# Performance work log

Hardware: AMD Instinct MI355X
Metric: run time of the kernel (lower is better)

## Reference

```python
import jax, jax.numpy as jnp
import numpy as np

SEQ, BATCH, IN, HID, OUT = 512, 64, 512, 1024, 512
KEEP = 0.7  # dropout p = 0.3


def setup_inputs() -> dict:
    key = jax.random.key(0)
    ks = jax.random.split(key, 9)
    def lin(k, fan_out, fan_in):
        bound = 1.0 / np.sqrt(fan_in)
        kw, kb = jax.random.split(k)
        W = jax.random.uniform(kw, (fan_out, fan_in), jnp.float32, -bound, bound)
        b = jax.random.uniform(kb, (fan_out,), jnp.float32, -bound, bound)
        return W, b
    x = jax.random.normal(ks[0], (SEQ, BATCH, IN), jnp.float32)
    # inverted dropout mask, fixed for determinism
    drop_mask = (jax.random.bernoulli(ks[1], KEEP, (SEQ, BATCH, OUT))
                 .astype(jnp.float32) / KEEP)
    W_i2h, b_i2h = lin(ks[2], HID, IN + HID)
    W_i2o, b_i2o = lin(ks[3], OUT, IN + HID)
    W_o2o, b_o2o = lin(ks[4], OUT, HID + OUT)
    return {"x": x, "drop_mask": drop_mask,
            "W_i2h": W_i2h, "b_i2h": b_i2h,
            "W_i2o": W_i2o, "b_i2o": b_i2o,
            "W_o2o": W_o2o, "b_o2o": b_o2o}


def reference(x, drop_mask, W_i2h, b_i2h, W_i2o, b_i2o, W_o2o, b_o2o):
    # x: [S, B, IN]; returns log-probs [S, B, OUT]
    def step(h, inp):
        x_t, m_t = inp  # [B, IN], [B, OUT]
        comb = jnp.concatenate([x_t, h], axis=1)          # [B, IN+HID]
        out = comb @ W_i2o.T + b_i2o                      # [B, OUT]
        h_new = comb @ W_i2h.T + b_i2h                    # [B, HID]
        oc = jnp.concatenate([out, h_new], axis=1) @ W_o2o.T + b_o2o  # [B, OUT]
        oc = oc * m_t                                     # dropout (inverted mask)
        oc = jax.nn.log_softmax(oc, axis=-1)
        return h_new, oc
    h0 = jnp.zeros((x.shape[1], W_i2h.shape[0]), x.dtype)
    _, outs = jax.lax.scan(step, h0, (x, drop_mask))
    return outs
```

## Files before the change

### kernel.cpp

```cpp
#include <hip/hip_runtime.h>
#include <stdint.h>
#include <string.h>


typedef unsigned short ushort_t;
typedef __attribute__((ext_vector_type(8))) __bf16 bf16x8;
typedef __attribute__((ext_vector_type(4))) float f32x4;

__device__ __forceinline__ ushort_t f2bf(float f) {
  union { float f; uint32_t u; } v; v.f = f;
  uint32_t r = v.u + 0x7fffu + ((v.u >> 16) & 1u);
  return (ushort_t)(r >> 16);
}
__device__ __forceinline__ float bf2f(ushort_t b) {
  union { uint32_t u; float f; } v; v.u = ((uint32_t)b) << 16;
  return v.f;
}

__global__ __launch_bounds__(256) void init_kernel(uint32_t* harr0) {
  int i = blockIdx.x * blockDim.x + threadIdx.x;
  if (i < 32768) harr0[i] = 0;
}

__global__ __launch_bounds__(256) void pack_kernel(
    const float* __restrict__ x, const float* __restrict__ W_i2h,
    const float* __restrict__ W_i2o, const float* __restrict__ W_o2o,
    ushort_t* xB, ushort_t* Wihx, ushort_t* Whh, ushort_t* Wiox,
    ushort_t* Wioh, ushort_t* Wo1, ushort_t* Wo2) {
  int64_t i = (int64_t)blockIdx.x * blockDim.x + threadIdx.x;
  const int64_t c0 = 16777216, c1 = 17301504, c2 = 18350080, c3 = 18612224,
                c4 = 19136512, c5 = 19398656, c6 = 19922944;
  if (i < c0) { xB[i] = f2bf(x[i]); return; }
  if (i < c1) { int64_t j = i - c0; int r = j >> 9,  c = j & 511;  Wihx[j] = f2bf(W_i2h[(int64_t)r * 1536 + c]); return; }
  if (i < c2) { int64_t j = i - c1; int r = j >> 10, c = j & 1023; Whh[j]  = f2bf(W_i2h[(int64_t)r * 1536 + 512 + c]); return; }
  if (i < c3) { int64_t j = i - c2; int r = j >> 9,  c = j & 511;  Wiox[j] = f2bf(W_i2o[(int64_t)r * 1536 + c]); return; }
  if (i < c4) { int64_t j = i - c3; int r = j >> 10, c = j & 1023; Wioh[j] = f2bf(W_i2o[(int64_t)r * 1536 + 512 + c]); return; }
  if (i < c5) { int64_t j = i - c4; int r = j >> 9,  c = j & 511;  Wo1[j]  = f2bf(W_o2o[(int64_t)r * 1536 + c]); return; }
  if (i < c6) { int64_t j = i - c5; int r = j >> 10, c = j & 1023; Wo2[j]  = f2bf(W_o2o[(int64_t)r * 1536 + 512 + c]); return; }
}

__global__ __launch_bounds__(256) void gemm_bt(
    const ushort_t* __restrict__ A1, int lda1, const ushort_t* __restrict__ B1, int K1,
    const ushort_t* __restrict__ A2, int lda2, const ushort_t* __restrict__ B2, int K2,
    const float* __restrict__ bias, float* Cf, ushort_t* Cb, int Ntiles) {
  __shared__ __align__(16) ushort_t As[128][32];
  __shared__ __align__(16) ushort_t Bs[128][32];
  const int mt = blockIdx.x / Ntiles, nt = blockIdx.x % Ntiles;
  const int m0 = mt * 128, n0 = nt * 128;
  const int tid = threadIdx.x;
  const int w = tid >> 6, l = tid & 63;
  const int quad = l >> 4, l15 = l & 15;
  const int wm = (w & 1) * 64, wn = (w >> 1) * 64;
  const int r0 = tid >> 2, chunk = tid & 3;
  f32x4 acc[4][4] = {};

  for (int phase = 0; phase < 2; ++phase) {
    const ushort_t* A = phase ? A2 : A1;
    const ushort_t* B = phase ? B2 : B1;
    const int lda = phase ? lda2 : lda1;
    const int K = phase ? K2 : K1;
    for (int k0 = 0; k0 < K; k0 += 32) {
      __syncthreads();
      *(uint4*)&As[r0][chunk * 8]      = *(const uint4*)(A + (size_t)(m0 + r0) * lda + k0 + chunk * 8);
      *(uint4*)&As[r0 + 64][chunk * 8] = *(const uint4*)(A + (size_t)(m0 + r0 + 64) * lda + k0 + chunk * 8);
      *(uint4*)&Bs[r0][chunk * 8]      = *(const uint4*)(B + (size_t)(n0 + r0) * K + k0 + chunk * 8);
      *(uint4*)&Bs[r0 + 64][chunk * 8] = *(const uint4*)(B + (size_t)(n0 + r0 + 64) * K + k0 + chunk * 8);
      __syncthreads();
      bf16x8 af[4], bfr[4];
#pragma unroll
      for (int i = 0; i < 4; ++i) af[i]  = *(const bf16x8*)&As[wm + 16 * i + l15][8 * quad];
#pragma unroll
      for (int j = 0; j < 4; ++j) bfr[j] = *(const bf16x8*)&Bs[wn + 16 * j + l15][8 * quad];
#pragma unroll
      for (int i = 0; i < 4; ++i)
#pragma unroll
        for (int j = 0; j < 4; ++j)
          acc[i][j] = __builtin_amdgcn_mfma_f32_16x16x32_bf16(af[i], bfr[j], acc[i][j], 0, 0, 0);
    }
  }

  const int N = Ntiles * 128;
#pragma unroll
  for (int i = 0; i < 4; ++i) {
    const int row = m0 + wm + 16 * i + 4 * quad;
#pragma unroll
    for (int j = 0; j < 4; ++j) {
      const int col = n0 + wn + 16 * j + l15;
      const float bv = bias[col];
#pragma unroll
      for (int r = 0; r < 4; ++r) {
        const float v = acc[i][j][r] + bv;
        const size_t idx = (size_t)(row + r) * N + col;
        if (Cf) Cf[idx] = v;
        else Cb[idx] = f2bf(v);
      }
    }
  }
}

__global__ __launch_bounds__(256) void gemm_bn(
    const ushort_t* __restrict__ Am, const ushort_t* __restrict__ Bm,
    ushort_t* __restrict__ Om) {
  __shared__ __align__(16) ushort_t As[128][32];
  __shared__ __align__(16) ushort_t Bs[128][32];
  const int mt = blockIdx.x >> 3, nt = blockIdx.x & 7;
  const int m0 = mt * 128, n0 = nt * 128;
  const int tid = threadIdx.x;
  const int w = tid >> 6, l = tid & 63;
  const int quad = l >> 4, l15 = l & 15;
  const int wm = (w & 1) * 64, wn = (w >> 1) * 64;
  const int r0 = tid >> 2, chunk = tid & 3;
  f32x4 acc[4][4] = {};
  for (int k0 = 0; k0 < 1024; k0 += 32) {
    __syncthreads();
    *(uint4*)&As[r0][chunk * 8]      = *(const uint4*)(Am + (size_t)(m0 + r0) * 1024 + k0 + chunk * 8);
    *(uint4*)&As[r0 + 64][chunk * 8] = *(const uint4*)(Am + (size_t)(m0 + r0 + 64) * 1024 + k0 + chunk * 8);
#pragma unroll
    for (int rep = 0; rep < 2; ++rep) {
      const int idx = tid + 256 * rep;
      const int kk = idx & 31, n8 = idx >> 5;
      union { uint4 v; ushort_t s[8]; } u;
      u.v = *(const uint4*)(Bm + (size_t)(k0 + kk) * 1024 + n0 + n8 * 8);
#pragma unroll
      for (int i = 0; i < 8; ++i) Bs[n8 * 8 + i][kk] = u.s[i];
    }
    __syncthreads();
    bf16x8 af[4], bfr[4];
#pragma unroll
    for (int i = 0; i < 4; ++i) af[i]  = *(const bf16x8*)&As[wm + 16 * i + l15][8 * quad];
#pragma unroll
    for (int j = 0; j < 4; ++j) bfr[j] = *(const bf16x8*)&Bs[wn + 16 * j + l15][8 * quad];
#pragma unroll
    for (int i = 0; i < 4; ++i)
#pragma unroll
      for (int j = 0; j < 4; ++j)
        acc[i][j] = __builtin_amdgcn_mfma_f32_16x16x32_bf16(af[i], bfr[j], acc[i][j], 0, 0, 0);
  }
#pragma unroll
  for (int i = 0; i < 4; ++i) {
    const int row = m0 + wm + 16 * i + 4 * quad;
#pragma unroll
    for (int j = 0; j < 4; ++j) {
      const int col = n0 + wn + 16 * j + l15;
#pragma unroll
      for (int r = 0; r < 4; ++r)
        Om[(size_t)(row + r) * 1024 + col] = f2bf(acc[i][j][r]);
    }
  }
}

__global__ __launch_bounds__(256) void rnn_step(
    const ushort_t* __restrict__ A, size_t aStride,
    const ushort_t* __restrict__ Xh, const ushort_t* __restrict__ Whh,
    ushort_t* __restrict__ O) {
  __shared__ __align__(16) ushort_t As[128][32];
  __shared__ __align__(16) ushort_t Bs[128][32];
  const int p = blockIdx.x >> 3;
  const int n0 = (blockIdx.x & 7) * 128;
  const int tid = threadIdx.x;
  const int w = tid >> 6, l = tid & 63;
  const int quad = l >> 4, l15 = l & 15;
  const int wm = (w & 1) * 64, wn = (w >> 1) * 64;
  const int r0 = tid >> 2, chunk = tid & 3;
  f32x4 acc[4][4] = {};
  const ushort_t* a0 = A + (size_t)(2 * p) * aStride + (size_t)r0 * 1024;
  const ushort_t* a1 = A + (size_t)(2 * p + 1) * aStride + (size_t)r0 * 1024;
  for (int k0 = 0; k0 < 1024; k0 += 32) {
    __syncthreads();
    *(uint4*)&As[r0][chunk * 8]      = *(const uint4*)(a0 + k0 + chunk * 8);
    *(uint4*)&As[r0 + 64][chunk * 8] = *(const uint4*)(a1 + k0 + chunk * 8);
    *(uint4*)&Bs[r0][chunk * 8]      = *(const uint4*)(Whh + (size_t)(n0 + r0) * 1024 + k0 + chunk * 8);
    *(uint4*)&Bs[r0 + 64][chunk * 8] = *(const uint4*)(Whh + (size_t)(n0 + r0 + 64) * 1024 + k0 + chunk * 8);
    __syncthreads();
    bf16x8 af[4], bfr[4];
#pragma unroll
    for (int i = 0; i < 4; ++i) af[i]  = *(const bf16x8*)&As[wm + 16 * i + l15][8 * quad];
#pragma unroll
    for (int j = 0; j < 4; ++j) bfr[j] = *(const bf16x8*)&Bs[wn + 16 * j + l15][8 * quad];
#pragma unroll
    for (int i = 0; i < 4; ++i)
#pragma unroll
      for (int j = 0; j < 4; ++j)
        acc[i][j] = __builtin_amdgcn_mfma_f32_16x16x32_bf16(af[i], bfr[j], acc[i][j], 0, 0, 0);
  }
#pragma unroll
  for (int i = 0; i < 4; ++i) {
#pragma unroll
    for (int j = 0; j < 4; ++j) {
      const int col = n0 + wn + 16 * j + l15;
#pragma unroll
      for (int r = 0; r < 4; ++r) {
        const int gr = wm + 16 * i + 4 * quad + r;
        const int c = 2 * p + (gr >> 6);
        const size_t idx = (size_t)c * 524288 + (size_t)(gr & 63) * 1024 + col;
        O[idx] = f2bf(acc[i][j][r] + bf2f(Xh[idx]));
      }
    }
  }
}

__global__ __launch_bounds__(256) void scan_step(
    const ushort_t* __restrict__ Sold, const ushort_t* __restrict__ V,
    ushort_t* __restrict__ Snew, int d) {
  __shared__ __align__(16) ushort_t As[128][32];
  __shared__ __align__(16) ushort_t Bs[128][32];
  const int p = blockIdx.x >> 3;
  const int n0 = (blockIdx.x & 7) * 128;
  const int tid = threadIdx.x;
  const int w = tid >> 6, l = tid & 63;
  const int quad = l >> 4, l15 = l & 15;
  const int wm = (w & 1) * 64, wn = (w >> 1) * 64;
  const int r0 = tid >> 2, chunk = tid & 3;
  f32x4 acc[4][4] = {};
  const int j0 = 2 * p, j1 = 2 * p + 1;
  const int s0 = (j0 >= d) ? j0 - d : j0;
  const int s1 = (j1 >= d) ? j1 - d : j1;
  const ushort_t* a0 = Sold + (size_t)s0 * 65536 + (size_t)r0 * 1024;
  const ushort_t* a1 = Sold + (size_t)s1 * 65536 + (size_t)r0 * 1024;
  for (int k0 = 0; k0 < 1024; k0 += 32) {
    __syncthreads();
    *(uint4*)&As[r0][chunk * 8]      = *(const uint4*)(a0 + k0 + chunk * 8);
    *(uint4*)&As[r0 + 64][chunk * 8] = *(const uint4*)(a1 + k0 + chunk * 8);
    *(uint4*)&Bs[r0][chunk * 8]      = *(const uint4*)(V + (size_t)(n0 + r0) * 1024 + k0 + chunk * 8);
    *(uint4*)&Bs[r0 + 64][chunk * 8] = *(const uint4*)(V + (size_t)(n0 + r0 + 64) * 1024 + k0 + chunk * 8);
    __syncthreads();
    bf16x8 af[4], bfr[4];
#pragma unroll
    for (int i = 0; i < 4; ++i) af[i]  = *(const bf16x8*)&As[wm + 16 * i + l15][8 * quad];
#pragma unroll
    for (int j = 0; j < 4; ++j) bfr[j] = *(const bf16x8*)&Bs[wn + 16 * j + l15][8 * quad];
#pragma unroll
    for (int i = 0; i < 4; ++i)
#pragma unroll
      for (int j = 0; j < 4; ++j)
        acc[i][j] = __builtin_amdgcn_mfma_f32_16x16x32_bf16(af[i], bfr[j], acc[i][j], 0, 0, 0);
  }
#pragma unroll
  for (int i = 0; i < 4; ++i) {
#pragma unroll
    for (int j = 0; j < 4; ++j) {
      const int col = n0 + wn + 16 * j + l15;
#pragma unroll
      for (int r = 0; r < 4; ++r) {
        const int gr = wm + 16 * i + 4 * quad + r;
        const int c = 2 * p + (gr >> 6);
        const size_t idx = (size_t)c * 65536 + (size_t)(gr & 63) * 1024 + col;
        const float g = (c >= d) ? acc[i][j][r] : 0.0f;
        Snew[idx] = f2bf(g + bf2f(Sold[idx]));
      }
    }
  }
}

__global__ __launch_bounds__(256) void copy_strided(
    ushort_t* __restrict__ dst, size_t dStride,
    const ushort_t* __restrict__ src, size_t sStride) {
  const int c = blockIdx.x >> 5, part = blockIdx.x & 31;
  const size_t off = (size_t)part * 2048 + (size_t)threadIdx.x * 8;
  *(uint4*)(dst + (size_t)c * dStride + off) = *(const uint4*)(src + (size_t)c * sStride + off);
}

__global__ __launch_bounds__(256) void softmax_kernel(
    float* __restrict__ out, const float* __restrict__ mask) {
  const int row = blockIdx.x;
  const int tid = threadIdx.x;
  const size_t base = (size_t)row * 512;
  __shared__ float sm[4], ss[4];
  const float v0 = out[base + tid] * mask[base + tid];
  const float v1 = out[base + tid + 256] * mask[base + tid + 256];
  float m = fmaxf(v0, v1);
#pragma unroll
  for (int off = 32; off; off >>= 1) m = fmaxf(m, __shfl_xor(m, off, 64));
  const int w = tid >> 6;
  if ((tid & 63) == 0) sm[w] = m;
  __syncthreads();
  m = fmaxf(fmaxf(sm[0], sm[1]), fmaxf(sm[2], sm[3]));
  float s = __expf(v0 - m) + __expf(v1 - m);
#pragma unroll
  for (int off = 32; off; off >>= 1) s += __shfl_xor(s, off, 64);
  if ((tid & 63) == 0) ss[w] = s;
  __syncthreads();
  s = ss[0] + ss[1] + ss[2] + ss[3];
  const float lg = logf(s);
  out[base + tid] = v0 - m - lg;
  out[base + tid + 256] = v1 - m - lg;
}

extern "C" void kernel_launch(void* const* d_in, const int* in_sizes, int n_in,
                              void* d_out, int out_size, void* d_ws, size_t ws_size,
                              hipStream_t stream) {
  const float* x     = (const float*)d_in[0];
  const float* mask  = (const float*)d_in[1];
  const float* W_i2h = (const float*)d_in[2];
  const float* b_i2h = (const float*)d_in[3];
  const float* W_i2o = (const float*)d_in[4];
  const float* b_i2o = (const float*)d_in[5];
  const float* W_o2o = (const float*)d_in[6];
  const float* b_o2o = (const float*)d_in[7];
  float* out = (float*)d_out;

  char* ws = (char*)d_ws;
  const size_t NEED = 207753216;
  if (ws_size < NEED) return;
  ushort_t* xB   = (ushort_t*)(ws + 0);
  ushort_t* XhB  = (ushort_t*)(ws + 33554432);
  ushort_t* Harr = (ushort_t*)(ws + 100663296);
  char* outbRegion = ws + 167903232;
  ushort_t* OUTB = (ushort_t*)outbRegion;
  ushort_t* SA   = (ushort_t*)(outbRegion + 0);
  ushort_t* SB   = (ushort_t*)(outbRegion + 8388608);
  ushort_t* P2   = (ushort_t*)(outbRegion + 0);
  ushort_t* P4   = (ushort_t*)(outbRegion + 2097152);
  ushort_t* P8   = (ushort_t*)(outbRegion + 16777216);
  ushort_t* P16  = (ushort_t*)(outbRegion + 18874368);
  ushort_t* P32  = (ushort_t*)(outbRegion + 20971520);
  ushort_t* P64  = (ushort_t*)(outbRegion + 23068672);
  ushort_t* P128 = (ushort_t*)(outbRegion + 25165824);
  ushort_t* P256 = (ushort_t*)(outbRegion + 27262976);
  ushort_t* Wihx = (ushort_t*)(ws + 201457664);
  ushort_t* Whh  = (ushort_t*)(ws + 202506240);
  ushort_t* Wiox = (ushort_t*)(ws + 204603392);
  ushort_t* Wioh = (ushort_t*)(ws + 205127680);
  ushort_t* Wo1  = (ushort_t*)(ws + 206176256);
  ushort_t* Wo2  = (ushort_t*)(ws + 206700544);

  hipLaunchKernelGGL(init_kernel, dim3(128), dim3(256), 0, stream, (uint32_t*)Harr);
  hipLaunchKernelGGL(pack_kernel, dim3(77824), dim3(256), 0, stream,
                     x, W_i2h, W_i2o, W_o2o, xB, Wihx, Whh, Wiox, Wioh, Wo1, Wo2);
  hipLaunchKernelGGL(gemm_bt, dim3(256 * 8), dim3(256), 0, stream,
                     xB, 512, Wihx, 512, (const ushort_t*)nullptr, 0,
                     (const ushort_t*)nullptr, 0, b_i2h, (float*)nullptr, XhB, 8);
  hipLaunchKernelGGL(gemm_bn, dim3(64), dim3(256), 0, stream, Whh, Whh, P2);
  hipLaunchKernelGGL(gemm_bn, dim3(64), dim3(256), 0, stream, P2, P2, P4);
  hipLaunchKernelGGL(gemm_bn, dim3(64), dim3(256), 0, stream, P4, P4, P8);
  hipLaunchKernelGGL(gemm_bn, dim3(64), dim3(256), 0, stream, P8, P8, P16);
  hipLaunchKernelGGL(gemm_bn, dim3(64), dim3(256), 0, stream, P16, P16, P32);
  hipLaunchKernelGGL(gemm_bn, dim3(64), dim3(256), 0, stream, P32, P32, P64);
  hipLaunchKernelGGL(gemm_bn, dim3(64), dim3(256), 0, stream, P64, P64, P128);
  hipLaunchKernelGGL(gemm_bn, dim3(64), dim3(256), 0, stream, P128, P128, P256);
  hipLaunchKernelGGL(copy_strided, dim3(2048), dim3(256), 0, stream,
                     Harr + 65536, (size_t)524288, XhB, (size_t)524288);
  for (int k = 1; k < 8; ++k)
    hipLaunchKernelGGL(rnn_step, dim3(256), dim3(256), 0, stream,
                       Harr + (size_t)k * 65536, (size_t)524288,
                       XhB + (size_t)k * 65536, Whh, Harr + (size_t)(k + 1) * 65536);
  hipLaunchKernelGGL(copy_strided, dim3(2048), dim3(256), 0, stream,
                     SA, (size_t)65536, Harr, (size_t)524288);
  hipLaunchKernelGGL(scan_step, dim3(256), dim3(256), 0, stream, SA, P8,   SB, 1);
  hipLaunchKernelGGL(scan_step, dim3(256), dim3(256), 0, stream, SB, P16,  SA, 2);
  hipLaunchKernelGGL(scan_step, dim3(256), dim3(256), 0, stream, SA, P32,  SB, 4);
  hipLaunchKernelGGL(scan_step, dim3(256), dim3(256), 0, stream, SB, P64,  SA, 8);
  hipLaunchKernelGGL(scan_step, dim3(256), dim3(256), 0, stream, SA, P128, SB, 16);
  hipLaunchKernelGGL(scan_step, dim3(256), dim3(256), 0, stream, SB, P256, SA, 32);
  hipLaunchKernelGGL(rnn_step, dim3(256), dim3(256), 0, stream,
                     SA, (size_t)65536, XhB, Whh, Harr + 65536);
  for (int k = 1; k < 8; ++k)
    hipLaunchKernelGGL(rnn_step, dim3(256), dim3(256), 0, stream,
                       Harr + (size_t)k * 65536, (size_t)524288,
                       XhB + (size_t)k * 65536, Whh, Harr + (size_t)(k + 1) * 65536);
  hipLaunchKernelGGL(gemm_bt, dim3(256 * 4), dim3(256), 0, stream,
                     xB, 512, Wiox, 512, Harr, 1024, Wioh, 1024,
                     b_i2o, (float*)nullptr, OUTB, 4);
  hipLaunchKernelGGL(gemm_bt, dim3(256 * 4), dim3(256), 0, stream,
                     OUTB, 512, Wo1, 512, Harr + 65536, 1024, Wo2, 1024,
                     b_o2o, out, (ushort_t*)nullptr, 4);
  hipLaunchKernelGGL(softmax_kernel, dim3(32768), dim3(256), 0, stream, out, mask);
}
```

Measured before the change: 1.270 ms.

## Replace sequential second-pass RNN steps with parallel power-corrected GEMM using direct LDS loads

```diff
diff --git a/kernel.cpp b/kernel.cpp
--- a/kernel.cpp
+++ b/kernel.cpp
@@ -1,6 +1,5 @@
 #include <hip/hip_runtime.h>
 #include <stdint.h>
-#include <string.h>
 
 
 typedef unsigned short ushort_t;
@@ -15,6 +14,12 @@
 __device__ __forceinline__ float bf2f(ushort_t b) {
   union { uint32_t u; float f; } v; v.u = ((uint32_t)b) << 16;
   return v.f;
+}
+
+__device__ __forceinline__ void gload16(const ushort_t* g, ushort_t* l) {
+  __builtin_amdgcn_global_load_lds(
+      (const __attribute__((address_space(1))) uint32_t*)g,
+      (__attribute__((address_space(3))) uint32_t*)l, 16, 0, 0);
 }
 
 __global__ __launch_bounds__(256) void init_kernel(uint32_t* harr0) {
@@ -43,9 +48,9 @@
     const ushort_t* __restrict__ A1, int lda1, const ushort_t* __restrict__ B1, int K1,
     const ushort_t* __restrict__ A2, int lda2, const ushort_t* __restrict__ B2, int K2,
     const float* __restrict__ bias, float* Cf, ushort_t* Cb, int Ntiles) {
-  __shared__ __align__(16) ushort_t As[128][32];
-  __shared__ __align__(16) ushort_t Bs[128][32];
-  const int mt = blockIdx.x / Ntiles, nt = blockIdx.x % Ntiles;
+  __shared__ __align__(16) ushort_t AsF[4096];
+  __shared__ __align__(16) ushort_t BsF[4096];
+  const int mt = blockIdx.x & 255, nt = blockIdx.x >> 8;
   const int m0 = mt * 128, n0 = nt * 128;
   const int tid = threadIdx.x;
   const int w = tid >> 6, l = tid & 63;
@@ -61,16 +66,16 @@
     const int K = phase ? K2 : K1;
     for (int k0 = 0; k0 < K; k0 += 32) {
       __syncthreads();
-      *(uint4*)&As[r0][chunk * 8]      = *(const uint4*)(A + (size_t)(m0 + r0) * lda + k0 + chunk * 8);
-      *(uint4*)&As[r0 + 64][chunk * 8] = *(const uint4*)(A + (size_t)(m0 + r0 + 64) * lda + k0 + chunk * 8);
-      *(uint4*)&Bs[r0][chunk * 8]      = *(const uint4*)(B + (size_t)(n0 + r0) * K + k0 + chunk * 8);
-      *(uint4*)&Bs[r0 + 64][chunk * 8] = *(const uint4*)(B + (size_t)(n0 + r0 + 64) * K + k0 + chunk * 8);
+      gload16(A + (size_t)(m0 + r0) * lda + k0 + chunk * 8,      &AsF[tid * 8]);
+      gload16(A + (size_t)(m0 + r0 + 64) * lda + k0 + chunk * 8, &AsF[2048 + tid * 8]);
+      gload16(B + (size_t)(n0 + r0) * K + k0 + chunk * 8,        &BsF[tid * 8]);
+      gload16(B + (size_t)(n0 + r0 + 64) * K + k0 + chunk * 8,   &BsF[2048 + tid * 8]);
       __syncthreads();
       bf16x8 af[4], bfr[4];
 #pragma unroll
-      for (int i = 0; i < 4; ++i) af[i]  = *(const bf16x8*)&As[wm + 16 * i + l15][8 * quad];
-#pragma unroll
-      for (int j = 0; j < 4; ++j) bfr[j] = *(const bf16x8*)&Bs[wn + 16 * j + l15][8 * quad];
+      for (int i = 0; i < 4; ++i) af[i]  = *(const bf16x8*)&AsF[(wm + 16 * i + l15) * 32 + 8 * quad];
+#pragma unroll
+      for (int j = 0; j < 4; ++j) bfr[j] = *(const bf16x8*)&BsF[(wn + 16 * j + l15) * 32 + 8 * quad];
 #pragma unroll
       for (int i = 0; i < 4; ++i)
 #pragma unroll
@@ -101,8 +106,8 @@
 __global__ __launch_bounds__(256) void gemm_bn(
     const ushort_t* __restrict__ Am, const ushort_t* __restrict__ Bm,
     ushort_t* __restrict__ Om) {
-  __shared__ __align__(16) ushort_t As[128][32];
-  __shared__ __align__(16) ushort_t Bs[128][32];
+  __shared__ __align__(16) ushort_t AsF[4096];
+  __shared__ __align__(16) ushort_t BsF[4096];
   const int mt = blockIdx.x >> 3, nt = blockIdx.x & 7;
   const int m0 = mt * 128, n0 = nt * 128;
   const int tid = threadIdx.x;
@@ -113,8 +118,8 @@
   f32x4 acc[4][4] = {};
   for (int k0 = 0; k0 < 1024; k0 += 32) {
     __syncthreads();
-    *(uint4*)&As[r0][chunk * 8]      = *(const uint4*)(Am + (size_t)(m0 + r0) * 1024 + k0 + chunk * 8);
-    *(uint4*)&As[r0 + 64][chunk * 8] = *(const uint4*)(Am + (size_t)(m0 + r0 + 64) * 1024 + k0 + chunk * 8);
+    gload16(Am + (size_t)(m0 + r0) * 1024 + k0 + chunk * 8,      &AsF[tid * 8]);
+    gload16(Am + (size_t)(m0 + r0 + 64) * 1024 + k0 + chunk * 8, &AsF[2048 + tid * 8]);
 #pragma unroll
     for (int rep = 0; rep < 2; ++rep) {
       const int idx = tid + 256 * rep;
@@ -122,14 +127,14 @@
       union { uint4 v; ushort_t s[8]; } u;
       u.v = *(const uint4*)(Bm + (size_t)(k0 + kk) * 1024 + n0 + n8 * 8);
 #pragma unroll
-      for (int i = 0; i < 8; ++i) Bs[n8 * 8 + i][kk] = u.s[i];
+      for (int i = 0; i < 8; ++i) BsF[(n8 * 8 + i) * 32 + kk] = u.s[i];
     }
     __syncthreads();
     bf16x8 af[4], bfr[4];
 #pragma unroll
-    for (int i = 0; i < 4; ++i) af[i]  = *(const bf16x8*)&As[wm + 16 * i + l15][8 * quad];
-#pragma unroll
-    for (int j = 0; j < 4; ++j) bfr[j] = *(const bf16x8*)&Bs[wn + 16 * j + l15][8 * quad];
+    for (int i = 0; i < 4; ++i) af[i]  = *(const bf16x8*)&AsF[(wm + 16 * i + l15) * 32 + 8 * quad];
+#pragma unroll
+    for (int j = 0; j < 4; ++j) bfr[j] = *(const bf16x8*)&BsF[(wn + 16 * j + l15) * 32 + 8 * quad];
 #pragma unroll
     for (int i = 0; i < 4; ++i)
 #pragma unroll
@@ -153,8 +158,8 @@
     const ushort_t* __restrict__ A, size_t aStride,
     const ushort_t* __restrict__ Xh, const ushort_t* __restrict__ Whh,
     ushort_t* __restrict__ O) {
-  __shared__ __align__(16) ushort_t As[128][32];
-  __shared__ __align__(16) ushort_t Bs[128][32];
+  __shared__ __align__(16) ushort_t AsF[4096];
+  __shared__ __align__(16) ushort_t BsF[4096];
   const int p = blockIdx.x >> 3;
   const int n0 = (blockIdx.x & 7) * 128;
   const int tid = threadIdx.x;
@@ -167,16 +172,16 @@
   const ushort_t* a1 = A + (size_t)(2 * p + 1) * aStride + (size_t)r0 * 1024;
   for (int k0 = 0; k0 < 1024; k0 += 32) {
     __syncthreads();
-    *(uint4*)&As[r0][chunk * 8]      = *(const uint4*)(a0 + k0 + chunk * 8);
-    *(uint4*)&As[r0 + 64][chunk * 8] = *(const uint4*)(a1 + k0 + chunk * 8);
-    *(uint4*)&Bs[r0][chunk * 8]      = *(const uint4*)(Whh + (size_t)(n0 + r0) * 1024 + k0 + chunk * 8);
-    *(uint4*)&Bs[r0 + 64][chunk * 8] = *(const uint4*)(Whh + (size_t)(n0 + r0 + 64) * 1024 + k0 + chunk * 8);
+    gload16(a0 + k0 + chunk * 8, &AsF[tid * 8]);
+    gload16(a1 + k0 + chunk * 8, &AsF[2048 + tid * 8]);
+    gload16(Whh + (size_t)(n0 + r0) * 1024 + k0 + chunk * 8,      &BsF[tid * 8]);
+    gload16(Whh + (size_t)(n0 + r0 + 64) * 1024 + k0 + chunk * 8, &BsF[2048 + tid * 8]);
     __syncthreads();
     bf16x8 af[4], bfr[4];
 #pragma unroll
-    for (int i = 0; i < 4; ++i) af[i]  = *(const bf16x8*)&As[wm + 16 * i + l15][8 * quad];
-#pragma unroll
-    for (int j = 0; j < 4; ++j) bfr[j] = *(const bf16x8*)&Bs[wn + 16 * j + l15][8 * quad];
+    for (int i = 0; i < 4; ++i) af[i]  = *(const bf16x8*)&AsF[(wm + 16 * i + l15) * 32 + 8 * quad];
+#pragma unroll
+    for (int j = 0; j < 4; ++j) bfr[j] = *(const bf16x8*)&BsF[(wn + 16 * j + l15) * 32 + 8 * quad];
 #pragma unroll
     for (int i = 0; i < 4; ++i)
 #pragma unroll
@@ -202,8 +207,8 @@
 __global__ __launch_bounds__(256) void scan_step(
     const ushort_t* __restrict__ Sold, const ushort_t* __restrict__ V,
     ushort_t* __restrict__ Snew, int d) {
-  __shared__ __align__(16) ushort_t As[128][32];
-  __shared__ __align__(16) ushort_t Bs[128][32];
+  __shared__ __align__(16) ushort_t AsF[4096];
+  __shared__ __align__(16) ushort_t BsF[4096];
   const int p = blockIdx.x >> 3;
   const int n0 = (blockIdx.x & 7) * 128;
   const int tid = threadIdx.x;
@@ -219,16 +224,16 @@
   const ushort_t* a1 = Sold + (size_t)s1 * 65536 + (size_t)r0 * 1024;
   for (int k0 = 0; k0 < 1024; k0 += 32) {
     __syncthreads();
-    *(uint4*)&As[r0][chunk * 8]      = *(const uint4*)(a0 + k0 + chunk * 8);
-    *(uint4*)&As[r0 + 64][chunk * 8] = *(const uint4*)(a1 + k0 + chunk * 8);
-    *(uint4*)&Bs[r0][chunk * 8]      = *(const uint4*)(V + (size_t)(n0 + r0) * 1024 + k0 + chunk * 8);
-    *(uint4*)&Bs[r0 + 64][chunk * 8] = *(const uint4*)(V + (size_t)(n0 + r0 + 64) * 1024 + k0 + chunk * 8);
+    gload16(a0 + k0 + chunk * 8, &AsF[tid * 8]);
+    gload16(a1 + k0 + chunk * 8, &AsF[2048 + tid * 8]);
+    gload16(V + (size_t)(n0 + r0) * 1024 + k0 + chunk * 8,      &BsF[tid * 8]);
+    gload16(V + (size_t)(n0 + r0 + 64) * 1024 + k0 + chunk * 8, &BsF[2048 + tid * 8]);
     __syncthreads();
     bf16x8 af[4], bfr[4];
 #pragma unroll
-    for (int i = 0; i < 4; ++i) af[i]  = *(const bf16x8*)&As[wm + 16 * i + l15][8 * quad];
-#pragma unroll
-    for (int j = 0; j < 4; ++j) bfr[j] = *(const bf16x8*)&Bs[wn + 16 * j + l15][8 * quad];
+    for (int i = 0; i < 4; ++i) af[i]  = *(const bf16x8*)&AsF[(wm + 16 * i + l15) * 32 + 8 * quad];
+#pragma unroll
+    for (int j = 0; j < 4; ++j) bfr[j] = *(const bf16x8*)&BsF[(wn + 16 * j + l15) * 32 + 8 * quad];
 #pragma unroll
     for (int i = 0; i < 4; ++i)
 #pragma unroll
@@ -247,6 +252,67 @@
         const size_t idx = (size_t)c * 65536 + (size_t)(gr & 63) * 1024 + col;
         const float g = (c >= d) ? acc[i][j][r] : 0.0f;
         Snew[idx] = f2bf(g + bf2f(Sold[idx]));
+      }
+    }
+  }
+}
+
+__global__ __launch_bounds__(256) void correct_kernel(
+    const ushort_t* __restrict__ S, ushort_t* __restrict__ Harr,
+    const ushort_t* __restrict__ B1, const ushort_t* __restrict__ B2,
+    const ushort_t* __restrict__ B3, const ushort_t* __restrict__ B4,
+    const ushort_t* __restrict__ B5, const ushort_t* __restrict__ B6,
+    const ushort_t* __restrict__ B7, const ushort_t* __restrict__ B8) {
+  __shared__ __align__(16) ushort_t AsF[4096];
+  __shared__ __align__(16) ushort_t BsF[4096];
+  const int p = blockIdx.x >> 3;
+  const int n0 = (blockIdx.x & 7) * 128;
+  const int j = blockIdx.y + 1;
+  const ushort_t* Wj;
+  switch (j) {
+    case 1: Wj = B1; break; case 2: Wj = B2; break;
+    case 3: Wj = B3; break; case 4: Wj = B4; break;
+    case 5: Wj = B5; break; case 6: Wj = B6; break;
+    case 7: Wj = B7; break; default: Wj = B8; break;
+  }
+  ushort_t* XO = Harr + (size_t)j * 65536;
+  const int tid = threadIdx.x;
+  const int w = tid >> 6, l = tid & 63;
+  const int quad = l >> 4, l15 = l & 15;
+  const int wm = (w & 1) * 64, wn = (w >> 1) * 64;
+  const int r0 = tid >> 2, chunk = tid & 3;
+  f32x4 acc[4][4] = {};
+  const ushort_t* a0 = S + (size_t)(2 * p) * 65536 + (size_t)r0 * 1024;
+  const ushort_t* a1 = S + (size_t)(2 * p + 1) * 65536 + (size_t)r0 * 1024;
+  for (int k0 = 0; k0 < 1024; k0 += 32) {
+    __syncthreads();
+    gload16(a0 + k0 + chunk * 8, &AsF[tid * 8]);
+    gload16(a1 + k0 + chunk * 8, &AsF[2048 + tid * 8]);
+    gload16(Wj + (size_t)(n0 + r0) * 1024 + k0 + chunk * 8,      &BsF[tid * 8]);
+    gload16(Wj + (size_t)(n0 + r0 + 64) * 1024 + k0 + chunk * 8, &BsF[2048 + tid * 8]);
+    __syncthreads();
+    bf16x8 af[4], bfr[4];
+#pragma unroll
+    for (int i = 0; i < 4; ++i) af[i]  = *(const bf16x8*)&AsF[(wm + 16 * i + l15) * 32 + 8 * quad];
+#pragma unroll
+    for (int jj = 0; jj < 4; ++jj) bfr[jj] = *(const bf16x8*)&BsF[(wn + 16 * jj + l15) * 32 + 8 * quad];
+#pragma unroll
+    for (int i = 0; i < 4; ++i)
+#pragma unroll
+      for (int jj = 0; jj < 4; ++jj)
+        acc[i][jj] = __builtin_amdgcn_mfma_f32_16x16x32_bf16(af[i], bfr[jj], acc[i][jj], 0, 0, 0);
+  }
+#pragma unroll
+  for (int i = 0; i < 4; ++i) {
+#pragma unroll
+    for (int jj = 0; jj < 4; ++jj) {
+      const int col = n0 + wn + 16 * jj + l15;
+#pragma unroll
+      for (int r = 0; r < 4; ++r) {
+        const int gr = wm + 16 * i + 4 * quad + r;
+        const int c = 2 * p + (gr >> 6);
+        const size_t idx = (size_t)c * 524288 + (size_t)(gr & 63) * 1024 + col;
+        XO[idx] = f2bf(acc[i][jj][r] + bf2f(XO[idx]));
       }
     }
   }
@@ -307,16 +373,13 @@
   ushort_t* Harr = (ushort_t*)(ws + 100663296);
   char* outbRegion = ws + 167903232;
   ushort_t* OUTB = (ushort_t*)outbRegion;
-  ushort_t* SA   = (ushort_t*)(outbRegion + 0);
-  ushort_t* SB   = (ushort_t*)(outbRegion + 8388608);
-  ushort_t* P2   = (ushort_t*)(outbRegion + 0);
-  ushort_t* P4   = (ushort_t*)(outbRegion + 2097152);
-  ushort_t* P8   = (ushort_t*)(outbRegion + 16777216);
-  ushort_t* P16  = (ushort_t*)(outbRegion + 18874368);
-  ushort_t* P32  = (ushort_t*)(outbRegion + 20971520);
-  ushort_t* P64  = (ushort_t*)(outbRegion + 23068672);
-  ushort_t* P128 = (ushort_t*)(outbRegion + 25165824);
-  ushort_t* P256 = (ushort_t*)(outbRegion + 27262976);
+  ushort_t* SA = (ushort_t*)(outbRegion + 0);
+  ushort_t* SB = (ushort_t*)(outbRegion + 8388608);
+  ushort_t* PB = (ushort_t*)(outbRegion + 16777216);
+  ushort_t* P2 = PB, *P4 = PB + 1048576, *P8 = PB + 2097152,
+          * S3 = PB + 3145728, *S5 = PB + 4194304, *S6 = PB + 5242880,
+          * S7 = PB + 6291456, *P256 = PB + 7340032;
+  ushort_t* P16 = S3, *P32 = S5, *P64 = S6, *P128 = S7;
   ushort_t* Wihx = (ushort_t*)(ws + 201457664);
   ushort_t* Whh  = (ushort_t*)(ws + 202506240);
   ushort_t* Wiox = (ushort_t*)(ws + 204603392);
@@ -327,7 +390,7 @@
   hipLaunchKernelGGL(init_kernel, dim3(128), dim3(256), 0, stream, (uint32_t*)Harr);
   hipLaunchKernelGGL(pack_kernel, dim3(77824), dim3(256), 0, stream,
                      x, W_i2h, W_i2o, W_o2o, xB, Wihx, Whh, Wiox, Wioh, Wo1, Wo2);
-  hipLaunchKernelGGL(gemm_bt, dim3(256 * 8), dim3(256), 0, stream,
+  hipLaunchKernelGGL(gemm_bt, dim3(2048), dim3(256), 0, stream,
                      xB, 512, Wihx, 512, (const ushort_t*)nullptr, 0,
                      (const ushort_t*)nullptr, 0, b_i2h, (float*)nullptr, XhB, 8);
   hipLaunchKernelGGL(gemm_bn, dim3(64), dim3(256), 0, stream, Whh, Whh, P2);
@@ -352,16 +415,16 @@
   hipLaunchKernelGGL(scan_step, dim3(256), dim3(256), 0, stream, SB, P64,  SA, 8);
   hipLaunchKernelGGL(scan_step, dim3(256), dim3(256), 0, stream, SA, P128, SB, 16);
   hipLaunchKernelGGL(scan_step, dim3(256), dim3(256), 0, stream, SB, P256, SA, 32);
-  hipLaunchKernelGGL(rnn_step, dim3(256), dim3(256), 0, stream,
-                     SA, (size_t)65536, XhB, Whh, Harr + 65536);
-  for (int k = 1; k < 8; ++k)
-    hipLaunchKernelGGL(rnn_step, dim3(256), dim3(256), 0, stream,
-                       Harr + (size_t)k * 65536, (size_t)524288,
-                       XhB + (size_t)k * 65536, Whh, Harr + (size_t)(k + 1) * 65536);
-  hipLaunchKernelGGL(gemm_bt, dim3(256 * 4), dim3(256), 0, stream,
+  hipLaunchKernelGGL(gemm_bn, dim3(64), dim3(256), 0, stream, Whh, P2, S3);
+  hipLaunchKernelGGL(gemm_bn, dim3(64), dim3(256), 0, stream, Whh, P4, S5);
+  hipLaunchKernelGGL(gemm_bn, dim3(64), dim3(256), 0, stream, P2,  P4, S6);
+  hipLaunchKernelGGL(gemm_bn, dim3(64), dim3(256), 0, stream, S3,  P4, S7);
+  hipLaunchKernelGGL(correct_kernel, dim3(256, 8), dim3(256), 0, stream,
+                     SA, Harr, Whh, P2, S3, P4, S5, S6, S7, P8);
+  hipLaunchKernelGGL(gemm_bt, dim3(1024), dim3(256), 0, stream,
                      xB, 512, Wiox, 512, Harr, 1024, Wioh, 1024,
                      b_i2o, (float*)nullptr, OUTB, 4);
-  hipLaunchKernelGGL(gemm_bt, dim3(256 * 4), dim3(256), 0, stream,
+  hipLaunchKernelGGL(gemm_bt, dim3(1024), dim3(256), 0, stream,
                      OUTB, 512, Wo1, 512, Harr + 65536, 1024, Wo2, 1024,
                      b_o2o, out, (ushort_t*)nullptr, 4);
   hipLaunchKernelGGL(softmax_kernel, dim3(32768), dim3(256), 0, stream, out, mask);
```

After: 1.254 ms. Within noise of the previous version (-1.3%).
